# Performance work log

Measured on AMD Instinct MI355X. Metric: run time of the kernel, lower is better.

## Reference

```python
import jax, jax.numpy as jnp
import numpy as np

UNITS = 50257
NEG = 8192
C = 2048
B, S = 2, 1024
LOG_RANGE = float(np.log(UNITS + 1.0))
ACC_HIT_NEG = -1e20  # stands in for TF's -FLOAT_MAX accidental-hit masking


def _log_uniform_prob(ids):
    # P(k) = (log(k+2) - log(k+1)) / log(range_max + 1)
    f = ids.astype(jnp.float32)
    return (jnp.log(f + 2.0) - jnp.log(f + 1.0)) / LOG_RANGE


def _expected_count(p):
    # expected count for unique log-uniform sampling with NEG draws
    return -jnp.expm1(NEG * jnp.log1p(-p))


def setup_inputs() -> dict:
    key = jax.random.key(0)
    k1, k2, k3, k4 = jax.random.split(key, 4)
    predictions = jax.random.normal(k1, (B, S, C), jnp.float32)
    targets = jax.random.randint(k2, (B, S), 0, UNITS, dtype=jnp.int32)
    kernel = jax.random.normal(k3, (C, UNITS), jnp.float32) * 0.02
    bias = jnp.zeros((UNITS,), jnp.float32)
    # log-uniform (Zipfian) negative samples, as in tf.random.log_uniform_candidate_sampler
    u = jax.random.uniform(k4, (NEG,), jnp.float32)
    sampled = jnp.clip(jnp.floor(jnp.exp(u * LOG_RANGE)).astype(jnp.int32) - 1, 0, UNITS - 1)
    return {"predictions": predictions, "targets": targets, "kernel": kernel,
            "bias": bias, "sampled": sampled}


def reference(predictions, targets, kernel, bias, sampled):
    x = predictions.reshape(-1, C)          # [N, C]
    t = targets.reshape(-1)                 # [N]
    n = x.shape[0]

    # full logits / softmax output (layer output)
    full_logits = x @ kernel + bias         # [N, UNITS]
    probs = jax.nn.softmax(full_logits, axis=-1)
    probs = probs.reshape(predictions.shape[:-1] + (UNITS,))

    # sampled softmax training loss (tf.nn.sampled_softmax_loss semantics)
    true_w = kernel.T[t]                    # [N, C] gather of true-class rows
    true_logit = jnp.sum(x * true_w, axis=-1) + bias[t] \
        - jnp.log(_expected_count(_log_uniform_prob(t)))            # [N]

    samp_logits = x @ kernel[:, sampled] + bias[sampled] \
        - jnp.log(_expected_count(_log_uniform_prob(sampled)))      # [N, NEG]

    # remove accidental hits (sampled class == true class)
    hits = sampled[None, :] == t[:, None]
    samp_logits = jnp.where(hits, ACC_HIT_NEG, samp_logits)

    all_logits = jnp.concatenate([true_logit[:, None], samp_logits], axis=1)  # [N, 1+NEG]
    per_ex = jax.nn.logsumexp(all_logits, axis=-1) - all_logits[:, 0]
    loss = jnp.mean(per_ex)  # Reduction.SUM_OVER_BATCH_SIZE

    return probs, loss
```

## Files before the change

### kernel.cpp

```cpp
#include <hip/hip_runtime.h>
#include <math.h>

#define UNITS 50257
#define UPAD  50304
#define NEG   8192
#define CDIM  2048
#define NROWS 2048
#define BM 128
#define BN 128
#define BK 32
#define LOG_RANGE_F 10.8249254f

typedef __attribute__((ext_vector_type(8))) short short8;
typedef __attribute__((ext_vector_type(4))) float floatx4;


__device__ __forceinline__ unsigned short f2b(float f) {
  unsigned int u = __float_as_uint(f);
  unsigned int lsb = (u >> 16) & 1u;
  u += 0x7fffu + lsb;
  return (unsigned short)(u >> 16);
}

__device__ __forceinline__ void async_copy16(const void* g, void* s) {
  __builtin_amdgcn_global_load_lds(
      (const __attribute__((address_space(1))) void*)g,
      (__attribute__((address_space(3))) void*)s, 16, 0, 0);
}

__device__ __forceinline__ float logq_of(int k) {
  float f = (float)k;
  float p = (logf(f + 2.0f) - logf(f + 1.0f)) / LOG_RANGE_F;
  float ec = -expm1f(8192.0f * log1pf(-p));
  return logf(ec);
}


__global__ void cvt_x_kernel(const float* __restrict__ x, unsigned short* __restrict__ xb) {
  int idx = blockIdx.x * 256 + threadIdx.x;
  float4 v = reinterpret_cast<const float4*>(x)[idx];
  unsigned long long r = (unsigned long long)f2b(v.x)
                       | ((unsigned long long)f2b(v.y) << 16)
                       | ((unsigned long long)f2b(v.z) << 32)
                       | ((unsigned long long)f2b(v.w) << 48);
  reinterpret_cast<unsigned long long*>(xb)[idx] = r;
}

__global__ void transposeW_kernel(const float* __restrict__ W, unsigned short* __restrict__ kT) {
  __shared__ float tile[32][33];
  int tx = threadIdx.x & 31, ty = threadIdx.x >> 5;
  int u0 = blockIdx.x * 32, k0 = blockIdx.y * 32;
  int u = u0 + tx;
#pragma unroll
  for (int r = 0; r < 4; r++) {
    int kk = ty + r * 8;
    tile[kk][tx] = (u < UNITS) ? W[(size_t)(k0 + kk) * UNITS + u] : 0.0f;
  }
  __syncthreads();
#pragma unroll
  for (int r = 0; r < 4; r++) {
    int uu = ty + r * 8;
    kT[(size_t)(u0 + uu) * CDIM + k0 + tx] = f2b(tile[tx][uu]);
  }
}

__global__ void gather_rows_kernel(const unsigned short* __restrict__ kT,
                                   const int* __restrict__ sampled,
                                   unsigned short* __restrict__ kTs) {
  int j = blockIdx.x;
  int s = sampled[j];
  const uint4* src = reinterpret_cast<const uint4*>(kT + (size_t)s * CDIM);
  uint4* dst = reinterpret_cast<uint4*>(kTs + (size_t)j * CDIM);
  dst[threadIdx.x] = src[threadIdx.x];
}

__global__ void prep_logq_kernel(const int* __restrict__ sampled, float* __restrict__ lqs) {
  int j = blockIdx.x * 256 + threadIdx.x;
  if (j < NEG) lqs[j] = logq_of(sampled[j]);
}

__global__ __launch_bounds__(256, 2)
void gemm_bt(const unsigned short* __restrict__ A, const unsigned short* __restrict__ B,
             float* __restrict__ Cc, const float* __restrict__ bias,
             const int* __restrict__ bidx, int nx, int ldc, int colsValid)
{
  __shared__ __align__(16) unsigned short As[BM * BK];
  __shared__ __align__(16) unsigned short Bs[BN * BK];

  int tid = threadIdx.x;
  int wave = tid >> 6, lane = tid & 63;

  int bid = blockIdx.x;
  const int GPC = 16;
  int panel = bid >> 8;
  int rem = bid & 255;
  int colsInPanel = nx - panel * GPC; if (colsInPanel > GPC) colsInPanel = GPC;
  int bx = panel * GPC + (rem % colsInPanel);
  int by = rem / colsInPanel;

  int m0 = by * BM;
  int n0 = bx * BN;

  int sIdx = wave * 2;
  int row0 = sIdx * 16 + (lane >> 2);
  int kc = (lane & 3) * 8;
  const unsigned short* gA = A + (size_t)(m0 + row0) * CDIM + kc;
  const unsigned short* gB = B + (size_t)(n0 + row0) * CDIM + kc;
  unsigned short* lA = As + sIdx * 512 + lane * 8;
  unsigned short* lB = Bs + sIdx * 512 + lane * 8;

  floatx4 acc[4][4];
#pragma unroll
  for (int i = 0; i < 4; i++)
#pragma unroll
    for (int j = 0; j < 4; j++) acc[i][j] = (floatx4){0.f, 0.f, 0.f, 0.f};

  int wm = wave >> 1, wn = wave & 1;
  int aRow = wm * 64 + (lane & 15);
  int bRow = wn * 64 + (lane & 15);
  int kf = (lane >> 4) * 8;

  for (int kt = 0; kt < CDIM / BK; ++kt) {
    int kk = kt * BK;
    async_copy16(gA + kk, lA);
    async_copy16(gA + (size_t)16 * CDIM + kk, lA + 512);
    async_copy16(gB + kk, lB);
    async_copy16(gB + (size_t)16 * CDIM + kk, lB + 512);
    __syncthreads();

    short8 af[4], bf[4];
#pragma unroll
    for (int mi = 0; mi < 4; mi++)
      af[mi] = *(const short8*)(As + (aRow + mi * 16) * BK + kf);
#pragma unroll
    for (int ni = 0; ni < 4; ni++)
      bf[ni] = *(const short8*)(Bs + (bRow + ni * 16) * BK + kf);
#pragma unroll
    for (int mi = 0; mi < 4; mi++)
#pragma unroll
      for (int ni = 0; ni < 4; ni++)
        acc[mi][ni] = __builtin_amdgcn_mfma_f32_16x16x32_bf16(af[mi], bf[ni], acc[mi][ni], 0, 0, 0);
    __syncthreads();
  }

  int rBase = m0 + wm * 64 + ((lane >> 4) << 2);
  int cBase = n0 + wn * 64 + (lane & 15);
#pragma unroll
  for (int mi = 0; mi < 4; mi++) {
#pragma unroll
    for (int ni = 0; ni < 4; ni++) {
      int gcol = cBase + ni * 16;
      if (gcol < colsValid) {
        float bv = bias[bidx ? bidx[gcol] : gcol];
#pragma unroll
        for (int v = 0; v < 4; v++) {
          int grow = rBase + mi * 16 + v;
          Cc[(size_t)grow * ldc + gcol] = acc[mi][ni][v] + bv;
        }
      }
    }
  }
}

__global__ void rownorm_kernel(float* __restrict__ logits, const int* __restrict__ targets,
                               float* __restrict__ true_logit)
{
  int i = blockIdx.x, tid = threadIdx.x;
  float* row = logits + (size_t)i * UNITS;
  int t = targets[i];
  __shared__ float red_m[4], red_s[4];

  float m = -INFINITY, s = 0.0f;
  for (int j = tid; j < UNITS; j += 256) {
    float v = row[j];
    if (j == t) true_logit[i] = v;
    float mn = fmaxf(m, v);
    s = s * __expf(m - mn) + __expf(v - mn);
    m = mn;
  }
#pragma unroll
  for (int o = 1; o < 64; o <<= 1) {
    float mo = __shfl_xor(m, o, 64);
    float so = __shfl_xor(s, o, 64);
    float mn = fmaxf(m, mo);
    s = s * __expf(m - mn) + so * __expf(mo - mn);
    m = mn;
  }
  int lane = tid & 63, wv = tid >> 6;
  if (lane == 0) { red_m[wv] = m; red_s[wv] = s; }
  __syncthreads();
  float M = fmaxf(fmaxf(red_m[0], red_m[1]), fmaxf(red_m[2], red_m[3]));
  float S = red_s[0] * __expf(red_m[0] - M) + red_s[1] * __expf(red_m[1] - M)
          + red_s[2] * __expf(red_m[2] - M) + red_s[3] * __expf(red_m[3] - M);
  float inv = 1.0f / S;
  for (int j = tid; j < UNITS; j += 256) {
    row[j] = __expf(row[j] - M) * inv;
  }
}

__global__ void loss_rows_kernel(const float* __restrict__ samp, const int* __restrict__ sampled,
                                 const float* __restrict__ lqs, const int* __restrict__ targets,
                                 const float* __restrict__ true_logit, float* __restrict__ per_ex)
{
  int i = blockIdx.x, tid = threadIdx.x;
  int t = targets[i];
  const float* row = samp + (size_t)i * NEG;
  float tq = true_logit[i] - logq_of(t);
  __shared__ float red[4];
  int lane = tid & 63, wv = tid >> 6;

  float m = tq;
  for (int j = tid; j < NEG; j += 256) {
    if (sampled[j] == t) continue;
    m = fmaxf(m, row[j] - lqs[j]);
  }
#pragma unroll
  for (int o = 32; o > 0; o >>= 1) m = fmaxf(m, __shfl_down(m, o, 64));
  if (lane == 0) red[wv] = m;
  __syncthreads();
  m = fmaxf(fmaxf(red[0], red[1]), fmaxf(red[2], red[3]));
  __syncthreads();

  float s = (tid == 0) ? __expf(tq - m) : 0.0f;
  for (int j = tid; j < NEG; j += 256) {
    if (sampled[j] == t) continue;
    s += __expf(row[j] - lqs[j] - m);
  }
#pragma unroll
  for (int o = 32; o > 0; o >>= 1) s += __shfl_down(s, o, 64);
  if (lane == 0) red[wv] = s;
  __syncthreads();
  if (tid == 0) per_ex[i] = m + logf(red[0] + red[1] + red[2] + red[3]) - tq;
}

__global__ void loss_final_kernel(const float* __restrict__ per_ex, float* __restrict__ out) {
  __shared__ float red[4];
  int tid = threadIdx.x;
  float s = 0.0f;
  for (int j = tid; j < NROWS; j += 256) s += per_ex[j];
#pragma unroll
  for (int o = 32; o > 0; o >>= 1) s += __shfl_down(s, o, 64);
  int lane = tid & 63, wv = tid >> 6;
  if (lane == 0) red[wv] = s;
  __syncthreads();
  if (tid == 0) out[0] = (red[0] + red[1] + red[2] + red[3]) * (1.0f / (float)NROWS);
}


extern "C" void kernel_launch(void* const* d_in, const int* in_sizes, int n_in,
                              void* d_out, int out_size, void* d_ws, size_t ws_size,
                              hipStream_t stream) {
  (void)in_sizes; (void)n_in; (void)out_size; (void)ws_size;
  const float* predictions = (const float*)d_in[0];
  const int*   targets     = (const int*)d_in[1];
  const float* W           = (const float*)d_in[2];
  const float* bias        = (const float*)d_in[3];
  const int*   sampled     = (const int*)d_in[4];
  float* out = (float*)d_out;

  char* ws = (char*)d_ws;
  size_t off = 0;
  unsigned short* xb  = (unsigned short*)(ws + off); off += (size_t)NROWS * CDIM * 2;
  unsigned short* kTs = (unsigned short*)(ws + off); off += (size_t)NEG * CDIM * 2;
  float* true_logit = (float*)(ws + off); off += (size_t)NROWS * 4;
  float* per_ex     = (float*)(ws + off); off += (size_t)NROWS * 4;
  float* lqs        = (float*)(ws + off); off += (size_t)NEG * 4;
  off = (off + 255) & ~(size_t)255;
  unsigned short* kT = (unsigned short*)(ws + off);
  float* samp = (float*)(ws + off);

  float* logits = out;

  cvt_x_kernel<<<(NROWS * CDIM / 4) / 256, 256, 0, stream>>>(predictions, xb);
  transposeW_kernel<<<dim3(UPAD / 32, CDIM / 32), 256, 0, stream>>>(W, kT);
  gather_rows_kernel<<<NEG, 256, 0, stream>>>(kT, sampled, kTs);
  prep_logq_kernel<<<NEG / 256, 256, 0, stream>>>(sampled, lqs);

  gemm_bt<<<(UPAD / BN) * (NROWS / BM), 256, 0, stream>>>(
      xb, kT, logits, bias, nullptr, UPAD / BN, UNITS, UNITS);
  gemm_bt<<<(NEG / BN) * (NROWS / BM), 256, 0, stream>>>(
      xb, kTs, samp, bias, sampled, NEG / BN, NEG, NEG);

  rownorm_kernel<<<NROWS, 256, 0, stream>>>(logits, targets, true_logit);
  loss_rows_kernel<<<NROWS, 256, 0, stream>>>(samp, sampled, lqs, targets, true_logit, per_ex);
  loss_final_kernel<<<1, 256, 0, stream>>>(per_ex, out + (size_t)NROWS * UNITS);
}
```

Before: 1.759 ms.

## Replace GEMM with 256x256 tiled, double-buffered, swizzled MFMA pipeline

Replaces the 128x128x32 single-buffered GEMM with a 512-thread 256x256x64 kernel. It double-buffers LDS with async global-to-LDS copies, XOR-swizzles the LDS layout to avoid bank conflicts, and interleaves staging of the next tiles with four MFMA phases using barriers and priority hints. The block-to-tile mapping is also changed to spread M-tiles across XCDs. This targets load stalls and low MFMA utilization in the dominant logits GEMM, at the cost of higher register and LDS pressure and a fragile hand-placed waitcnt schedule.

Result: faster. 1.660 ms (-5.7%).

```diff
diff --git a/kernel.cpp b/kernel.cpp
--- a/kernel.cpp
+++ b/kernel.cpp
@@ -3,13 +3,17 @@
 
 #define UNITS 50257
 #define UPAD  50304
+#define NCT   197
 #define NEG   8192
 #define CDIM  2048
 #define NROWS 2048
-#define BM 128
-#define BN 128
-#define BK 32
 #define LOG_RANGE_F 10.8249254f
+
+#define BM2 256
+#define BN2 256
+#define BK2 64
+#define ASZ (256 * 64)
+#define NT2 (CDIM / BK2)
 
 typedef __attribute__((ext_vector_type(8))) short short8;
 typedef __attribute__((ext_vector_type(4))) float floatx4;
@@ -79,74 +83,165 @@
   if (j < NEG) lqs[j] = logq_of(sampled[j]);
 }
 
-__global__ __launch_bounds__(256, 2)
-void gemm_bt(const unsigned short* __restrict__ A, const unsigned short* __restrict__ B,
+
+__device__ __forceinline__ void stage_half(unsigned short* ldsHalf,
+                                           const unsigned short* gMat, int rowBase,
+                                           size_t kByteOff, int maxRow,
+                                           int wave, int lane) {
+#pragma unroll
+  for (int i = 0; i < 2; i++) {
+    int rl = i * 64 + wave * 8 + (lane >> 3);
+    int gr = rowBase + rl;
+    if (gr >= maxRow) gr = maxRow - 1;
+    const char* g = (const char*)(gMat + (size_t)gr * CDIM) + kByteOff
+                  + (((lane & 7) ^ (lane >> 3)) << 4);
+    unsigned short* s = ldsHalf + (size_t)(i * 64 + wave * 8) * 64 + lane * 8;
+    async_copy16(g, s);
+  }
+}
+
+#define PH_PRE() do { \
+    __builtin_amdgcn_s_barrier(); \
+    asm volatile("s_waitcnt lgkmcnt(0)" ::: "memory"); \
+    __builtin_amdgcn_sched_barrier(0); \
+    __builtin_amdgcn_s_setprio(1); \
+  } while (0)
+#define PH_POST() do { \
+    __builtin_amdgcn_s_setprio(0); \
+    __builtin_amdgcn_s_barrier(); \
+    __builtin_amdgcn_sched_barrier(0); \
+  } while (0)
+
+__global__ __launch_bounds__(512, 2)
+void gemm256(const unsigned short* __restrict__ A, const unsigned short* __restrict__ B,
              float* __restrict__ Cc, const float* __restrict__ bias,
-             const int* __restrict__ bidx, int nx, int ldc, int colsValid)
+             const int* __restrict__ bidx, int bRows, int ldc, int colsValid)
 {
-  __shared__ __align__(16) unsigned short As[BM * BK];
-  __shared__ __align__(16) unsigned short Bs[BN * BK];
-
-  int tid = threadIdx.x;
-  int wave = tid >> 6, lane = tid & 63;
-
-  int bid = blockIdx.x;
-  const int GPC = 16;
-  int panel = bid >> 8;
-  int rem = bid & 255;
-  int colsInPanel = nx - panel * GPC; if (colsInPanel > GPC) colsInPanel = GPC;
-  int bx = panel * GPC + (rem % colsInPanel);
-  int by = rem / colsInPanel;
-
-  int m0 = by * BM;
-  int n0 = bx * BN;
-
-  int sIdx = wave * 2;
-  int row0 = sIdx * 16 + (lane >> 2);
-  int kc = (lane & 3) * 8;
-  const unsigned short* gA = A + (size_t)(m0 + row0) * CDIM + kc;
-  const unsigned short* gB = B + (size_t)(n0 + row0) * CDIM + kc;
-  unsigned short* lA = As + sIdx * 512 + lane * 8;
-  unsigned short* lB = Bs + sIdx * 512 + lane * 8;
-
-  floatx4 acc[4][4];
-#pragma unroll
-  for (int i = 0; i < 4; i++)
+  __shared__ __align__(16) unsigned short lds[4 * ASZ];
+
+  const int tid = threadIdx.x;
+  const int wave = tid >> 6, lane = tid & 63;
+  const int wm = wave >> 2, wn = wave & 3;
+
+  const int qq = (int)gridDim.x >> 3;
+  const int wg = ((int)blockIdx.x & 7) * qq + ((int)blockIdx.x >> 3);
+  const int m0 = (wg & 7) * BM2;
+  const int n0 = (wg >> 3) * BN2;
+
+  const int fr = lane & 15;
+  const int cs0 = 8 * ((lane >> 4) ^ (lane & 7));
+  const int aRowBase = wm * 128 + fr;
+  const int bRowBase = wn * 64 + fr;
+
+  floatx4 acc[8][4];
+#pragma unroll
+  for (int i = 0; i < 8; i++)
 #pragma unroll
     for (int j = 0; j < 4; j++) acc[i][j] = (floatx4){0.f, 0.f, 0.f, 0.f};
-
-  int wm = wave >> 1, wn = wave & 1;
-  int aRow = wm * 64 + (lane & 15);
-  int bRow = wn * 64 + (lane & 15);
-  int kf = (lane >> 4) * 8;
-
-  for (int kt = 0; kt < CDIM / BK; ++kt) {
-    int kk = kt * BK;
-    async_copy16(gA + kk, lA);
-    async_copy16(gA + (size_t)16 * CDIM + kk, lA + 512);
-    async_copy16(gB + kk, lB);
-    async_copy16(gB + (size_t)16 * CDIM + kk, lB + 512);
-    __syncthreads();
-
-    short8 af[4], bf[4];
-#pragma unroll
-    for (int mi = 0; mi < 4; mi++)
-      af[mi] = *(const short8*)(As + (aRow + mi * 16) * BK + kf);
-#pragma unroll
-    for (int ni = 0; ni < 4; ni++)
-      bf[ni] = *(const short8*)(Bs + (bRow + ni * 16) * BK + kf);
-#pragma unroll
-    for (int mi = 0; mi < 4; mi++)
-#pragma unroll
-      for (int ni = 0; ni < 4; ni++)
-        acc[mi][ni] = __builtin_amdgcn_mfma_f32_16x16x32_bf16(af[mi], bf[ni], acc[mi][ni], 0, 0, 0);
-    __syncthreads();
-  }
-
-  int rBase = m0 + wm * 64 + ((lane >> 4) << 2);
-  int cBase = n0 + wn * 64 + (lane & 15);
-#pragma unroll
-  for (int mi = 0; mi < 4; mi++) {
+  short8 aF[8][2], bF[4][2];
+
+  {
+    unsigned short* A0b = lds;
+    unsigned short* A1b = lds + ASZ;
+    unsigned short* B0b = lds + 2 * ASZ;
+    stage_half(A0b,            A, m0,       0, NROWS, wave, lane);
+    stage_half(A0b + 128 * 64, A, m0 + 128, 0, NROWS, wave, lane);
+    stage_half(B0b,            B, n0,       0, bRows, wave, lane);
+    stage_half(B0b + 128 * 64, B, n0 + 128, 0, bRows, wave, lane);
+    stage_half(A1b,            A, m0,       BK2 * 2, NROWS, wave, lane);
+    stage_half(A1b + 128 * 64, A, m0 + 128, BK2 * 2, NROWS, wave, lane);
+    asm volatile("s_waitcnt vmcnt(4)" ::: "memory");
+    __builtin_amdgcn_sched_barrier(0);
+    __builtin_amdgcn_s_barrier();
+  }
+
+#pragma unroll 1
+  for (int t = 0; t < NT2; ++t) {
+    unsigned short* Ab = lds + ((t & 1) ? ASZ : 0);
+    unsigned short* Bb = lds + 2 * ASZ + ((t & 1) ? ASZ : 0);
+    unsigned short* Bn = lds + 2 * ASZ + ((t & 1) ? 0 : ASZ);
+    size_t kNext = (size_t)(t + 1) * BK2 * 2;
+    size_t kNext2 = (size_t)(t + 2) * BK2 * 2;
+
+#pragma unroll
+    for (int mi = 0; mi < 4; ++mi) {
+      int ra = (aRowBase + mi * 16) * 64;
+      aF[mi][0] = *(const short8*)(Ab + ra + cs0);
+      aF[mi][1] = *(const short8*)(Ab + ra + (cs0 ^ 32));
+    }
+#pragma unroll
+    for (int ni = 0; ni < 2; ++ni) {
+      int rb = (bRowBase + ni * 16) * 64;
+      bF[ni][0] = *(const short8*)(Bb + rb + cs0);
+      bF[ni][1] = *(const short8*)(Bb + rb + (cs0 ^ 32));
+    }
+    if (t + 1 < NT2) stage_half(Bn, B, n0, kNext, bRows, wave, lane);
+    PH_PRE();
+#pragma unroll
+    for (int mi = 0; mi < 4; ++mi)
+#pragma unroll
+      for (int ni = 0; ni < 2; ++ni) {
+        acc[mi][ni] = __builtin_amdgcn_mfma_f32_16x16x32_bf16(aF[mi][0], bF[ni][0], acc[mi][ni], 0, 0, 0);
+        acc[mi][ni] = __builtin_amdgcn_mfma_f32_16x16x32_bf16(aF[mi][1], bF[ni][1], acc[mi][ni], 0, 0, 0);
+      }
+    PH_POST();
+
+#pragma unroll
+    for (int mi = 4; mi < 8; ++mi) {
+      int ra = (aRowBase + mi * 16) * 64;
+      aF[mi][0] = *(const short8*)(Ab + ra + cs0);
+      aF[mi][1] = *(const short8*)(Ab + ra + (cs0 ^ 32));
+    }
+    if (t + 1 < NT2) stage_half(Bn + 128 * 64, B, n0 + 128, kNext, bRows, wave, lane);
+    PH_PRE();
+#pragma unroll
+    for (int mi = 4; mi < 8; ++mi)
+#pragma unroll
+      for (int ni = 0; ni < 2; ++ni) {
+        acc[mi][ni] = __builtin_amdgcn_mfma_f32_16x16x32_bf16(aF[mi][0], bF[ni][0], acc[mi][ni], 0, 0, 0);
+        acc[mi][ni] = __builtin_amdgcn_mfma_f32_16x16x32_bf16(aF[mi][1], bF[ni][1], acc[mi][ni], 0, 0, 0);
+      }
+    PH_POST();
+
+#pragma unroll
+    for (int ni = 2; ni < 4; ++ni) {
+      int rb = (bRowBase + ni * 16) * 64;
+      bF[ni][0] = *(const short8*)(Bb + rb + cs0);
+      bF[ni][1] = *(const short8*)(Bb + rb + (cs0 ^ 32));
+    }
+    if (t + 2 < NT2) stage_half(Ab, A, m0, kNext2, NROWS, wave, lane);
+    PH_PRE();
+#pragma unroll
+    for (int mi = 0; mi < 4; ++mi)
+#pragma unroll
+      for (int ni = 2; ni < 4; ++ni) {
+        acc[mi][ni] = __builtin_amdgcn_mfma_f32_16x16x32_bf16(aF[mi][0], bF[ni][0], acc[mi][ni], 0, 0, 0);
+        acc[mi][ni] = __builtin_amdgcn_mfma_f32_16x16x32_bf16(aF[mi][1], bF[ni][1], acc[mi][ni], 0, 0, 0);
+      }
+    PH_POST();
+
+    if (t + 2 < NT2) {
+      stage_half(Ab + 128 * 64, A, m0 + 128, kNext2, NROWS, wave, lane);
+      asm volatile("s_waitcnt vmcnt(4)" ::: "memory");
+    } else {
+      asm volatile("s_waitcnt vmcnt(0)" ::: "memory");
+    }
+    __builtin_amdgcn_sched_barrier(0);
+    PH_PRE();
+#pragma unroll
+    for (int mi = 4; mi < 8; ++mi)
+#pragma unroll
+      for (int ni = 2; ni < 4; ++ni) {
+        acc[mi][ni] = __builtin_amdgcn_mfma_f32_16x16x32_bf16(aF[mi][0], bF[ni][0], acc[mi][ni], 0, 0, 0);
+        acc[mi][ni] = __builtin_amdgcn_mfma_f32_16x16x32_bf16(aF[mi][1], bF[ni][1], acc[mi][ni], 0, 0, 0);
+      }
+    PH_POST();
+  }
+
+  int rBase = m0 + wm * 128 + ((lane >> 4) << 2);
+  int cBase = n0 + wn * 64 + fr;
+#pragma unroll
+  for (int mi = 0; mi < 8; mi++) {
 #pragma unroll
     for (int ni = 0; ni < 4; ni++) {
       int gcol = cBase + ni * 16;
@@ -161,6 +256,7 @@
     }
   }
 }
+
 
 __global__ void rownorm_kernel(float* __restrict__ logits, const int* __restrict__ targets,
                                float* __restrict__ true_logit)
@@ -276,10 +372,10 @@
   gather_rows_kernel<<<NEG, 256, 0, stream>>>(kT, sampled, kTs);
   prep_logq_kernel<<<NEG / 256, 256, 0, stream>>>(sampled, lqs);
 
-  gemm_bt<<<(UPAD / BN) * (NROWS / BM), 256, 0, stream>>>(
-      xb, kT, logits, bias, nullptr, UPAD / BN, UNITS, UNITS);
-  gemm_bt<<<(NEG / BN) * (NROWS / BM), 256, 0, stream>>>(
-      xb, kTs, samp, bias, sampled, NEG / BN, NEG, NEG);
+  gemm256<<<NCT * (NROWS / BM2), 512, 0, stream>>>(
+      xb, kT, logits, bias, nullptr, UPAD, UNITS, UNITS);
+  gemm256<<<(NEG / BN2) * (NROWS / BM2), 512, 0, stream>>>(
+      xb, kTs, samp, bias, sampled, NEG, NEG, NEG);
 
   rownorm_kernel<<<NROWS, 256, 0, stream>>>(logits, targets, true_logit);
   loss_rows_kernel<<<NROWS, 256, 0, stream>>>(samp, sampled, lqs, targets, true_logit, per_ex);
```
